# Kernel optimization log

Hardware: AMD Instinct MI355X
Metric: run time of the kernel (lower is better)

## Reference

```python
import jax, jax.numpy as jnp
import numpy as np

A = 9
H = 384
W = 384
MIN_SIZE = 2.0
NMS_THRESH = 0.7
PRE_NMS = 6000
POST_NMS = 300


def _make_anchors():
    # anchors.generate_anchors((H, W), box_sizes): per-cell (x1, y1, w, h) boxes in
    # feature-map coordinates, one box per (anchor, y, x).
    sizes = []
    for s in (4.0, 8.0, 16.0):
        for r in (0.5, 1.0, 2.0):
            sizes.append((s * np.sqrt(r), s / np.sqrt(r)))
    ys, xs = np.meshgrid(np.arange(H, dtype=np.float32), np.arange(W, dtype=np.float32), indexing='ij')
    cx, cy = xs + 0.5, ys + 0.5
    anch = np.stack([
        np.stack([cx - w / 2, cy - h / 2, np.full_like(cx, w), np.full_like(cx, h)], axis=-1)
        for (w, h) in sizes
    ], axis=0)  # [A, H, W, 4]
    return jnp.asarray(anch, jnp.float32)


def setup_inputs() -> dict:
    key = jax.random.key(0)
    k1, k2 = jax.random.split(key)
    scores = jax.random.uniform(k1, (1, A, H, W), dtype=jnp.float32)
    bbox_deltas = jax.random.normal(k2, (1, 4 * A, H, W), dtype=jnp.float32)
    return {
        'scores': scores,
        'bbox_deltas': bbox_deltas,
        'anchor_boxes': _make_anchors(),
        'image_metadata': jnp.zeros((1, 3), jnp.float32),
    }


def _clip_boxes(boxes, length, width):
    # clip_boxes_batch: clamp everything to >=0, convert (x,y,w,h)->(x1,y1,x2,y2),
    # clip to feature-map bounds, convert back.
    b = jnp.maximum(boxes, 0.0)
    x1, y1, w, h = b[..., 0], b[..., 1], b[..., 2], b[..., 3]
    x2 = x1 + w - 1.0
    y2 = y1 + h - 1.0
    x1 = jnp.minimum(x1, length - 1.0)
    y1 = jnp.minimum(y1, width - 1.0)
    x2 = jnp.minimum(x2, length - 1.0)
    y2 = jnp.minimum(y2, width - 1.0)
    return jnp.stack([x1, y1, x2 - x1 + 1.0, y2 - y1 + 1.0], axis=-1)


def _nms(boxes, valid):
    # Faithful port of the source's sequential NMS: repeatedly pick the remaining
    # box with the largest y2, suppress boxes whose intersection / own-area >= thresh.
    x1, y1, w, h = boxes[:, 0], boxes[:, 1], boxes[:, 2], boxes[:, 3]
    x2 = x1 + w - 1.0
    y2 = y1 + h - 1.0
    areas = w * h
    NEG = jnp.float32(-1e30)

    def cond(st):
        v, keep, cnt = st
        return (cnt < POST_NMS) & jnp.any(v)

    def body(st):
        v, keep, cnt = st
        ind = jnp.argmax(jnp.where(v, y2, NEG))
        xx1 = jnp.maximum(x1, x1[ind])
        yy1 = jnp.maximum(y1, y1[ind])
        xx2 = jnp.minimum(x2, x2[ind])
        yy2 = jnp.minimum(y2, y2[ind])
        inter = jnp.maximum(xx2 - xx1 + 1.0, 0.0) * jnp.maximum(yy2 - yy1 + 1.0, 0.0)
        ratio = inter / areas  # intersection over each candidate's own area (as in source)
        nv = v & (ratio < NMS_THRESH)
        nv = nv.at[ind].set(False)
        return nv, keep.at[cnt].set(ind.astype(jnp.int32)), cnt + 1

    keep0 = jnp.full((POST_NMS,), -1, jnp.int32)
    _, keep, cnt = jax.lax.while_loop(cond, body, (valid, keep0, jnp.int32(0)))
    return keep, cnt


def reference(scores, bbox_deltas, anchor_boxes, image_metadata):
    B = 1
    _, _, Hh, Ww = scores.shape
    # two contiguous .view()s compose to a single reshape
    deltas = bbox_deltas.reshape(B, A, Hh, Ww, 4)
    boxes = anchor_boxes[None] + deltas               # [1, A, H, W, 4]
    clipped = _clip_boxes(boxes, float(Hh), float(Ww))
    keep = (clipped[..., 2] >= MIN_SIZE) & (clipped[..., 3] >= MIN_SIZE)

    N = A * Hh * Ww
    boxes_f = clipped.reshape(N, 4)
    scores_f = scores.reshape(N)
    masked = jnp.where(keep.reshape(N), scores_f, jnp.float32(-jnp.inf))

    # descending score sort, PRE_NMS_TOP_N truncation
    order = jnp.argsort(-masked)[:PRE_NMS]
    props = boxes_f[order]                            # [PRE_NMS, 4]
    sc = masked[order]
    valid = jnp.isfinite(sc)

    keep_idx, cnt = _nms(props, valid)
    sel = props[jnp.maximum(keep_idx, 0)]             # [POST_NMS, 4]
    slot_valid = jnp.arange(POST_NMS) < cnt
    out = jnp.where(slot_valid[:, None], sel, 0.0)[None]  # [1, POST_NMS, 4]
    return out
```

## Files before the change

### kernel.cpp

```cpp
#include <hip/hip_runtime.h>
#include <stdint.h>

#define NN 1327104
#define NQ 331776
#define NB 1296
#define PRE_NMS_ 6000
#define POST_NMS_ 300
#define LB_CAP 4096
#define NPAD 6144
#define NWORD 96
#define KB 16
#define MATB 192


static __device__ __forceinline__ uint32_t score_key(float s) {
  uint32_t b = __float_as_uint(s);
  uint32_t u = b ^ (((int32_t)b < 0) ? 0xFFFFFFFFu : 0x80000000u);
  return ~u;
}

static __device__ __forceinline__ uint32_t f2s(float v) {
  uint32_t b = __float_as_uint(v);
  return b ^ (((int32_t)b < 0) ? 0xFFFFFFFFu : 0x80000000u);
}

static __device__ __forceinline__ void compute_box(float4 an, float4 de,
    float& x1, float& y1, float& wc, float& hc, bool& keep) {
  float bx = fmaxf(an.x + de.x, 0.0f);
  float by = fmaxf(an.y + de.y, 0.0f);
  float bw = fmaxf(an.z + de.z, 0.0f);
  float bh = fmaxf(an.w + de.w, 0.0f);
  float x2 = bx + bw - 1.0f;
  float y2 = by + bh - 1.0f;
  x1 = fminf(bx, 383.0f);
  y1 = fminf(by, 383.0f);
  x2 = fminf(x2, 383.0f);
  y2 = fminf(y2, 383.0f);
  wc = x2 - x1 + 1.0f;
  hc = y2 - y1 + 1.0f;
  keep = (wc >= 2.0f) && (hc >= 2.0f);
}

static __device__ __forceinline__ uint32_t kb18_of(float s) {
  return (uint32_t)(s * 262144.0f);
}

static __device__ __forceinline__ uint32_t wscan(uint32_t v, int l) {
  #pragma unroll
  for (int off = 1; off < 64; off <<= 1) {
    uint32_t u = __shfl_up(v, off);
    if (l >= off) v += u;
  }
  return v;
}

static __device__ __forceinline__ void pick1_f(const uint32_t* __restrict__ h1,
                                               uint32_t& selR8, uint32_t& base1) {
  int l = threadIdx.x & 63;
  uint32_t a0 = h1[l*5], a1 = h1[l*5+1], a2 = h1[l*5+2], a3 = h1[l*5+3], a4 = h1[l*5+4];
  uint32_t c0 = a0, c1 = c0+a1, c2 = c1+a2, c3 = c2+a3, c4 = c3+a4;
  uint32_t inc = wscan(c4, l);
  uint32_t excl = inc - c4;
  bool hit = (excl < PRE_NMS_) && (inc >= PRE_NMS_);
  unsigned long long hb = __ballot(hit);
  int hl = __ffsll(hb) - 1;
  uint32_t k, cb;
  if      (excl + c0 >= PRE_NMS_) { k = 0; cb = 0;  }
  else if (excl + c1 >= PRE_NMS_) { k = 1; cb = c0; }
  else if (excl + c2 >= PRE_NMS_) { k = 2; cb = c1; }
  else if (excl + c3 >= PRE_NMS_) { k = 3; cb = c2; }
  else                            { k = 4; cb = c3; }
  selR8 = __shfl(l*5u + k, hl);
  base1 = __shfl(excl + cb, hl);
}

static __device__ __forceinline__ void pick2_f(const uint32_t* __restrict__ h2,
                                               uint32_t base1,
                                               uint32_t& selR10, uint32_t& C0) {
  int l = threadIdx.x & 63;
  const uint4* p = (const uint4*)(h2 + l * 16);
  uint4 va = p[0], vb = p[1], vc = p[2], vd = p[3];
  uint32_t h[16] = {va.x,va.y,va.z,va.w, vb.x,vb.y,vb.z,vb.w,
                    vc.x,vc.y,vc.z,vc.w, vd.x,vd.y,vd.z,vd.w};
  uint32_t cum[16]; cum[0] = h[0];
  #pragma unroll
  for (int k = 1; k < 16; ++k) cum[k] = cum[k-1] + h[k];
  uint32_t inc = wscan(cum[15], l);
  uint32_t excl = base1 + inc - cum[15];
  bool hit = (excl < PRE_NMS_) && (base1 + inc >= PRE_NMS_);
  unsigned long long hb = __ballot(hit);
  int hl = __ffsll(hb) - 1;
  uint32_t k = 15, cb = cum[14];
  #pragma unroll
  for (int kk = 15; kk >= 0; --kk)
    if (excl + cum[kk] >= PRE_NMS_) { k = (uint32_t)kk; cb = kk ? cum[kk-1] : 0u; }
  selR10 = __shfl(l*16u + k, hl);
  C0 = __shfl(excl + cb, hl);
}

__global__ __launch_bounds__(256) void k_hA(const float* __restrict__ scores,
                                            const float4* __restrict__ deltas,
                                            const float4* __restrict__ anchors,
                                            uint32_t* __restrict__ darr,
                                            uint32_t* __restrict__ hist1,
                                            uint32_t* __restrict__ zpad) {
  __shared__ uint32_t lh[320];
  int t = threadIdx.x;
  for (int j = t; j < 320; j += 256) lh[j] = 0;
  __syncthreads();
  int base = blockIdx.x * 256 + t;
  #pragma unroll
  for (int it = 0; it < 4; ++it) {
    int i = base + it * NQ;
    float x1, y1, wc, hc; bool keep;
    compute_box(anchors[i], deltas[i], x1, y1, wc, hc, keep);
    float s = scores[i];
    uint32_t d = keep ? score_key(s) : 0xFF800000u;
    darr[i] = d;
    uint32_t r8 = keep ? (255u - (kb18_of(s) >> 10)) : 256u;
    atomicAdd(&lh[r8], 1u);
  }
  __syncthreads();
  for (int j = t; j < 320; j += 256) {
    uint32_t c = lh[j];
    if (c) atomicAdd(&hist1[j], c);
  }
  if (blockIdx.x == 0) for (int j = t; j < 1024 + 16 + 128; j += 256) zpad[j] = 0;
}

__global__ __launch_bounds__(256) void k_hB(const uint4* __restrict__ dv,
                                            const uint32_t* __restrict__ hist1,
                                            uint32_t* __restrict__ hist2) {
  __shared__ uint32_t lh2[1024];
  int t = threadIdx.x;
  uint32_t selR8, base1;
  pick1_f(hist1, selR8, base1);
  for (int j = t; j < 1024; j += 256) lh2[j] = 0;
  __syncthreads();
  uint4 v = dv[blockIdx.x * 256 + t];
  uint32_t arr[4] = {v.x, v.y, v.z, v.w};
  #pragma unroll
  for (int k = 0; k < 4; ++k) {
    uint32_t d = arr[k];
    if (d <= 0x7FFFFFFFu) {
      uint32_t kb = kb18_of(__uint_as_float(0x7FFFFFFFu - d));
      if ((255u - (kb >> 10)) == selR8) atomicAdd(&lh2[1023u - (kb & 1023u)], 1u);
    } else if (selR8 == 256u) {
      atomicAdd(&lh2[0], 1u);
    }
  }
  __syncthreads();
  for (int j = t; j < 1024; j += 256) {
    uint32_t c = lh2[j];
    if (c) atomicAdd(&hist2[j], c);
  }
}

__global__ __launch_bounds__(256) void k_gather(const uint4* __restrict__ dv,
                                                const uint32_t* __restrict__ hist1,
                                                const uint32_t* __restrict__ hist2,
                                                uint32_t* __restrict__ ctr,
                                                uint64_t* __restrict__ L,
                                                uint64_t* __restrict__ Lb) {
  __shared__ uint32_t s_sel8, s_sel10;
  int t = threadIdx.x;
  if (t < 64) {
    uint32_t sel8, base1, sel10, c0;
    pick1_f(hist1, sel8, base1);
    pick2_f(hist2, base1, sel10, c0);
    if (t == 0) { s_sel8 = sel8; s_sel10 = sel10; }
  }
  __syncthreads();
  uint32_t selR8 = s_sel8, selR10 = s_sel10;
  int g = blockIdx.x * 256 + t;
  uint4 v = dv[g];
  uint32_t arr[4] = {v.x, v.y, v.z, v.w};
  #pragma unroll
  for (int k = 0; k < 4; ++k) {
    uint32_t d = arr[k];
    uint32_t idx = (uint32_t)(g * 4 + k);
    bool above = false, boundary = false;
    if (d <= 0x7FFFFFFFu) {
      uint32_t kb = kb18_of(__uint_as_float(0x7FFFFFFFu - d));
      uint32_t r8 = 255u - (kb >> 10), r10 = 1023u - (kb & 1023u);
      above = (r8 < selR8) || (r8 == selR8 && r10 < selR10);
      boundary = (r8 == selR8) && (r10 == selR10);
    } else {
      boundary = (selR8 == 256u) && (selR10 == 0u);
    }
    if (above) {
      uint32_t p = atomicAdd(&ctr[0], 1u);
      if (p < PRE_NMS_) L[p] = ((uint64_t)d << 32) | idx;
    } else if (boundary) {
      uint32_t p = atomicAdd(&ctr[1], 1u);
      if (p < LB_CAP) Lb[p] = ((uint64_t)d << 32) | idx;
    }
  }
}

__global__ __launch_bounds__(256) void k_prep(const uint32_t* __restrict__ hist1,
                                              const uint32_t* __restrict__ hist2,
                                              const uint32_t* __restrict__ ctr,
                                              const uint64_t* __restrict__ L,
                                              const uint64_t* __restrict__ Lb,
                                              const float4* __restrict__ deltas,
                                              const float4* __restrict__ anchors,
                                              uint64_t* __restrict__ keyhi,
                                              uint32_t* __restrict__ keylo,
                                              float4* __restrict__ box4u) {
  uint32_t sel8, base1, sel10, C0;
  pick1_f(hist1, sel8, base1);
  pick2_f(hist2, base1, sel10, C0);
  int i = blockIdx.x * 256 + threadIdx.x;
  if (i >= NPAD) return;
  if (i < PRE_NMS_) {
    uint64_t mykey;
    if ((uint32_t)i < C0) {
      mykey = L[i];
    } else {
      uint32_t Cb = ctr[1]; if (Cb > LB_CAP) Cb = LB_CAP;
      uint32_t r = (uint32_t)i - C0;
      mykey = ~0ULL;
      for (uint32_t j = 0; j < Cb; ++j) {
        uint64_t kj = Lb[j];
        uint32_t rj = 0;
        for (uint32_t k = 0; k < Cb; ++k) rj += (Lb[k] < kj) ? 1u : 0u;
        if (rj == r) { mykey = kj; break; }
      }
    }
    uint32_t d = (uint32_t)(mykey >> 32), idx = (uint32_t)mykey;
    float x1, y1, wc, hc; bool keep;
    compute_box(anchors[idx], deltas[idx], x1, y1, wc, hc, keep);
    float y2 = y1 + hc - 1.0f;
    keyhi[i] = ((uint64_t)f2s(y2) << 32) | (uint32_t)(~d);
    keylo[i] = ~idx;
    box4u[i] = make_float4(x1, y1, wc, hc);
  } else {
    keyhi[i] = 0;
    keylo[i] = (uint32_t)(NPAD - i);
    box4u[i] = make_float4(0.f, 0.f, 0.f, 0.f);
  }
}

__global__ __launch_bounds__(512) void k_rank(const uint64_t* __restrict__ keyhi,
                                              const uint32_t* __restrict__ keylo,
                                              uint32_t* __restrict__ rank2d) {
  __shared__ uint64_t shi[768];
  __shared__ uint32_t slo[768];
  int t = threadIdx.x;
  int ib = blockIdx.x >> 3, c = blockIdx.x & 7, base = c * 768;
  for (int j = t; j < 768; j += 512) { shi[j] = keyhi[base + j]; slo[j] = keylo[base + j]; }
  __syncthreads();
  int i = ib * 256 + (t >> 1);
  int h = t & 1;
  uint64_t hi = keyhi[i]; uint32_t lo = keylo[i];
  uint32_t cnt = 0;
  int j0 = h * 384;
  for (int j = j0; j < j0 + 384; ++j) {
    uint64_t hj = shi[j]; uint32_t lj = slo[j];
    cnt += ((hj > hi) || (hj == hi && lj > lo)) ? 1u : 0u;
  }
  rank2d[i * 16 + c * 2 + h] = cnt;
}

#define FOR16(F) F(0) F(1) F(2) F(3) F(4) F(5) F(6) F(7) \
                 F(8) F(9) F(10) F(11) F(12) F(13) F(14) F(15)

static __device__ void seq_body(const unsigned long long* __restrict__ valid,
    const uint64_t* __restrict__ M, const float4* __restrict__ sobox,
    float* __restrict__ out, int* __restrict__ cslot) {
  int l = threadIdx.x;
  unsigned long long v0 = valid[l];
  unsigned long long v1 = (l < 32) ? valid[64 + l] : 0ull;
  uint32_t cnt = 0;

  for (;;) {
    uint32_t n0 = (uint32_t)__popcll(v0);
    uint32_t inc0 = wscan(n0, l);
    uint32_t T0 = __shfl(inc0, 63);
    uint32_t ex0 = inc0 - n0;
    uint32_t n1 = (uint32_t)__popcll(v1);
    uint32_t inc1 = wscan(n1, l);
    uint32_t T1 = __shfl(inc1, 63);
    uint32_t ex1 = T0 + inc1 - n1;
    uint32_t TV = T0 + T1;
    if (cnt >= POST_NMS_ || TV == 0) break;
    uint32_t m = (TV < KB) ? TV : KB;

    if (l < KB) cslot[l] = 0;
    __builtin_amdgcn_sched_barrier(0);
    if (ex0 < KB) {
      unsigned long long w = v0; uint32_t r = ex0;
      while (w && r < KB) { int b = __ffsll(w) - 1; cslot[r] = l * 64 + b; ++r; w &= w - 1; }
    }
    if (ex1 < KB && v1) {
      unsigned long long w = v1; uint32_t r = ex1;
      while (w && r < KB) { int b = __ffsll(w) - 1; cslot[r] = (64 + l) * 64 + b; ++r; w &= w - 1; }
    }
    __builtin_amdgcn_sched_barrier(0);

#define ROWDECL(k) uint64_t rm0_##k = 0, rm1_##k = 0;
    FOR16(ROWDECL)
#undef ROWDECL
#define ROWLOAD(k) if (k < (int)m) { const uint64_t* p = M + (size_t)cslot[k] * NWORD; \
                     rm0_##k = p[l]; rm1_##k = (l < 32) ? p[64 + l] : 0ull; }
    FOR16(ROWLOAD)
#undef ROWLOAD
    float4 obox = make_float4(0.f, 0.f, 0.f, 0.f);
    if (l < KB) obox = sobox[cslot[l]];

    uint32_t cj = (l < KB) ? (uint32_t)cslot[l] : 0u;
    uint32_t wj = cj >> 6, bj = cj & 63;
    int srcA = (int)(wj & 63), srcB = (int)(wj & 31);
    uint32_t srow[KB];
#define SROW(k) { uint64_t a = __shfl((unsigned long long)rm0_##k, srcA); \
                  uint64_t b = __shfl((unsigned long long)rm1_##k, srcB); \
                  uint64_t sel = (wj < 64) ? a : b; \
                  uint32_t bit = (l < KB && k < (int)m) ? (uint32_t)((sel >> bj) & 1) : 0u; \
                  srow[k] = (uint32_t)(__ballot(bit) & 0xFFFFull); }
    FOR16(SROW)
#undef SROW

    uint32_t cnt0 = cnt;
    uint32_t wm = 0, supp = 0;
    #pragma unroll
    for (int k = 0; k < KB; ++k) {
      if (k < (int)m && cnt < POST_NMS_ && !((supp >> k) & 1)) {
        wm |= 1u << k; ++cnt; supp |= srow[k];
      }
    }

    if (l < KB && ((wm >> l) & 1)) {
      uint32_t pos = cnt0 + (uint32_t)__popc(wm & ((1u << l) - 1));
      *(float4*)(out + (size_t)pos * 4) = obox;
    }

    uint64_t comb0 = 0, comb1 = 0;
#define COMB(k) if ((wm >> k) & 1) { comb0 |= rm0_##k; comb1 |= rm1_##k; }
    FOR16(COMB)
#undef COMB
    v0 &= ~comb0; v1 &= ~comb1;
  }

  for (int j = l; j < (int)(POST_NMS_ - cnt) * 4; j += 64) out[cnt * 4 + j] = 0.0f;
}

__global__ __launch_bounds__(512) void k_matsc(const uint64_t* __restrict__ keyhi,
                                               const uint32_t* __restrict__ rank2d,
                                               const float4* __restrict__ box4u,
                                               float4* __restrict__ sobox,
                                               unsigned long long* __restrict__ valid,
                                               uint64_t* __restrict__ M,
                                               uint32_t* __restrict__ ctr,
                                               float* __restrict__ out) {
  __shared__ float4 sb[NPAD];
  __shared__ float  sa[NPAD];
  __shared__ int    cslot[KB];
  __shared__ uint32_t lastf;
  int t = threadIdx.x;
  int b = blockIdx.x;
  for (int i = t; i < NPAD; i += 512) {
    const uint4* rp = (const uint4*)(rank2d + (size_t)i * 16);
    uint4 r0 = rp[0], r1 = rp[1], r2 = rp[2], r3 = rp[3];
    uint32_t r = r0.x+r0.y+r0.z+r0.w + r1.x+r1.y+r1.z+r1.w
               + r2.x+r2.y+r2.z+r2.w + r3.x+r3.y+r3.z+r3.w;
    float4 bx = box4u[i];
    float x2 = bx.x + bx.z - 1.0f;
    float y2 = bx.y + bx.w - 1.0f;
    sb[r] = make_float4(bx.x, bx.y, x2, y2);
    sa[r] = bx.z * bx.w;
    if (b == 0) {
      sobox[r] = bx;
      uint32_t d = ~(uint32_t)(keyhi[i] & 0xFFFFFFFFu);
      if (d < 0xFF800000u)
        atomicOr(&valid[r >> 6], 1ull << (r & 63));
    }
  }
  __syncthreads();
  int wid = t >> 6, l = t & 63;
  #pragma unroll
  for (int rr = 0; rr < 4; ++rr) {
    int r = b * 32 + wid * 4 + rr;
    float4 rb = sb[r];
    for (int w = 0; w < NWORD; ++w) {
      int j = w * 64 + l;
      float4 cb = sb[j];
      float ca = sa[j];
      float xx1 = fmaxf(cb.x, rb.x), yy1 = fmaxf(cb.y, rb.y);
      float xx2 = fminf(cb.z, rb.z), yy2 = fminf(cb.w, rb.w);
      float iw = fmaxf(xx2 - xx1 + 1.0f, 0.0f);
      float ih = fmaxf(yy2 - yy1 + 1.0f, 0.0f);
      float ratio = (iw * ih) / ca;
      unsigned long long mm = __ballot(!(ratio < 0.7f));
      if (l == 0) M[(size_t)r * NWORD + w] = mm;
    }
  }
  __syncthreads();
  __threadfence();
  if (t == 0) lastf = (atomicAdd(&ctr[8], 1u) == (uint32_t)(gridDim.x - 1)) ? 1u : 0u;
  __syncthreads();
  if (lastf) {
    __threadfence();
    if (t < 64) seq_body(valid, M, sobox, out, cslot);
  }
}

extern "C" void kernel_launch(void* const* d_in, const int* in_sizes, int n_in,
                              void* d_out, int out_size, void* d_ws, size_t ws_size,
                              hipStream_t stream) {
  const float*  scores  = (const float*)d_in[0];
  const float4* deltas  = (const float4*)d_in[1];
  const float4* anchors = (const float4*)d_in[2];
  float* out = (float*)d_out;

  uint8_t* w8 = (uint8_t*)d_ws;
  uint32_t* darr  = (uint32_t*)w8;
  uint64_t* M     = (uint64_t*)w8;
  float4*   sobox = (float4*)(w8 + 4841472);
  uint64_t* keyhi  = (uint64_t*)(w8 + 5308416);
  uint32_t* keylo  = (uint32_t*)(w8 + 5357568);
  float4*   box4u  = (float4*)  (w8 + 5382144);
  uint32_t* rank2d = (uint32_t*)(w8 + 5480448);
  uint32_t* hist1 = (uint32_t*)(w8 + 5873664);
  uint32_t* hist2 = (uint32_t*)(w8 + 5874944);
  uint32_t* ctr   = (uint32_t*)(w8 + 5879040);
  unsigned long long* valid = (unsigned long long*)(w8 + 5879104);
  uint64_t* L    = (uint64_t*)(w8 + 5880128);
  uint64_t* Lb   = (uint64_t*)(w8 + 5928128);

  const uint4* dv = (const uint4*)darr;

  hipMemsetAsync(hist1, 0, 1280, stream);

  k_hA    <<<NB, 256, 0, stream>>>(scores, deltas, anchors, darr, hist1, hist2);
  k_hB    <<<NB, 256, 0, stream>>>(dv, hist1, hist2);
  k_gather<<<NB, 256, 0, stream>>>(dv, hist1, hist2, ctr, L, Lb);
  k_prep  <<<NPAD / 256, 256, 0, stream>>>(hist1, hist2, ctr, L, Lb, deltas, anchors,
                                           keyhi, keylo, box4u);
  k_rank  <<<MATB, 512, 0, stream>>>(keyhi, keylo, rank2d);
  k_matsc <<<MATB, 512, 0, stream>>>(keyhi, rank2d, box4u, sobox, valid, M, ctr, out);
}
```

Measured before the change: 311.8 us.

## Fold second histogram pass and prep into gather, split sequential NMS kernel

Removes the second full-array histogram kernel and the separate prep kernel. The gather kernel now collects the whole 8-bit boundary bucket, and the last block builds the 10-bit histogram from that small list, picks the threshold, and emits keys and boxes directly. The quadratic rank search over the Lb list is replaced by a second-level select plus a small shared-memory rank among at most 256 items. The sequential NMS stage moves to its own 1024-thread kernel, where extra waves stream over the mask matrix to warm cache and the main wave raises its priority. The risks are a last-block serial tail, a larger boundary capacity whose overflow would give wrong results, and the bnd cap of 256.

```diff
diff --git a/kernel.cpp b/kernel.cpp
--- a/kernel.cpp
+++ b/kernel.cpp
@@ -6,7 +6,7 @@
 #define NB 1296
 #define PRE_NMS_ 6000
 #define POST_NMS_ 300
-#define LB_CAP 4096
+#define LB_CAP 16384
 #define NPAD 6144
 #define NWORD 96
 #define KB 16
@@ -74,28 +74,39 @@
   base1 = __shfl(excl + cb, hl);
 }
 
-static __device__ __forceinline__ void pick2_f(const uint32_t* __restrict__ h2,
-                                               uint32_t base1,
-                                               uint32_t& selR10, uint32_t& C0) {
+static __device__ __forceinline__ void pickT_lds(const uint32_t* __restrict__ h2,
+                                                 uint32_t T,
+                                                 uint32_t& sel10, uint32_t& base) {
   int l = threadIdx.x & 63;
-  const uint4* p = (const uint4*)(h2 + l * 16);
-  uint4 va = p[0], vb = p[1], vc = p[2], vd = p[3];
-  uint32_t h[16] = {va.x,va.y,va.z,va.w, vb.x,vb.y,vb.z,vb.w,
-                    vc.x,vc.y,vc.z,vc.w, vd.x,vd.y,vd.z,vd.w};
+  uint32_t h[16];
+  #pragma unroll
+  for (int k = 0; k < 16; ++k) h[k] = h2[l*16 + k];
   uint32_t cum[16]; cum[0] = h[0];
   #pragma unroll
   for (int k = 1; k < 16; ++k) cum[k] = cum[k-1] + h[k];
   uint32_t inc = wscan(cum[15], l);
-  uint32_t excl = base1 + inc - cum[15];
-  bool hit = (excl < PRE_NMS_) && (base1 + inc >= PRE_NMS_);
+  uint32_t excl = inc - cum[15];
+  bool hit = (excl < T) && (inc >= T);
   unsigned long long hb = __ballot(hit);
   int hl = __ffsll(hb) - 1;
   uint32_t k = 15, cb = cum[14];
   #pragma unroll
   for (int kk = 15; kk >= 0; --kk)
-    if (excl + cum[kk] >= PRE_NMS_) { k = (uint32_t)kk; cb = kk ? cum[kk-1] : 0u; }
-  selR10 = __shfl(l*16u + k, hl);
-  C0 = __shfl(excl + cb, hl);
+    if (excl + cum[kk] >= T) { k = (uint32_t)kk; cb = kk ? cum[kk-1] : 0u; }
+  sel10 = __shfl(l*16u + k, hl);
+  base  = __shfl(excl + cb, hl);
+}
+
+static __device__ __forceinline__ void emit_item(uint32_t pos, uint32_t d, uint32_t idx,
+    const float4* __restrict__ deltas, const float4* __restrict__ anchors,
+    uint64_t* __restrict__ keyhi, uint32_t* __restrict__ keylo,
+    float4* __restrict__ box4u) {
+  float x1, y1, wc, hc; bool keep;
+  compute_box(anchors[idx], deltas[idx], x1, y1, wc, hc, keep);
+  float y2 = y1 + hc - 1.0f;
+  keyhi[pos] = ((uint64_t)f2s(y2) << 32) | (uint32_t)(~d);
+  keylo[pos] = ~idx;
+  box4u[pos] = make_float4(x1, y1, wc, hc);
 }
 
 __global__ __launch_bounds__(256) void k_hA(const float* __restrict__ scores,
@@ -103,7 +114,7 @@
                                             const float4* __restrict__ anchors,
                                             uint32_t* __restrict__ darr,
                                             uint32_t* __restrict__ hist1,
-                                            uint32_t* __restrict__ zpad) {
+                                            uint32_t* __restrict__ zctr) {
   __shared__ uint32_t lh[320];
   int t = threadIdx.x;
   for (int j = t; j < 320; j += 256) lh[j] = 0;
@@ -125,53 +136,29 @@
     uint32_t c = lh[j];
     if (c) atomicAdd(&hist1[j], c);
   }
-  if (blockIdx.x == 0) for (int j = t; j < 1024 + 16 + 128; j += 256) zpad[j] = 0;
-}
-
-__global__ __launch_bounds__(256) void k_hB(const uint4* __restrict__ dv,
-                                            const uint32_t* __restrict__ hist1,
-                                            uint32_t* __restrict__ hist2) {
-  __shared__ uint32_t lh2[1024];
-  int t = threadIdx.x;
-  uint32_t selR8, base1;
-  pick1_f(hist1, selR8, base1);
-  for (int j = t; j < 1024; j += 256) lh2[j] = 0;
-  __syncthreads();
-  uint4 v = dv[blockIdx.x * 256 + t];
-  uint32_t arr[4] = {v.x, v.y, v.z, v.w};
-  #pragma unroll
-  for (int k = 0; k < 4; ++k) {
-    uint32_t d = arr[k];
-    if (d <= 0x7FFFFFFFu) {
-      uint32_t kb = kb18_of(__uint_as_float(0x7FFFFFFFu - d));
-      if ((255u - (kb >> 10)) == selR8) atomicAdd(&lh2[1023u - (kb & 1023u)], 1u);
-    } else if (selR8 == 256u) {
-      atomicAdd(&lh2[0], 1u);
-    }
-  }
-  __syncthreads();
-  for (int j = t; j < 1024; j += 256) {
-    uint32_t c = lh2[j];
-    if (c) atomicAdd(&hist2[j], c);
-  }
+  if (blockIdx.x == 0) for (int j = t; j < 272; j += 256) zctr[j] = 0;
 }
 
 __global__ __launch_bounds__(256) void k_gather(const uint4* __restrict__ dv,
                                                 const uint32_t* __restrict__ hist1,
-                                                const uint32_t* __restrict__ hist2,
                                                 uint32_t* __restrict__ ctr,
-                                                uint64_t* __restrict__ L,
-                                                uint64_t* __restrict__ Lb) {
-  __shared__ uint32_t s_sel8, s_sel10;
+                                                uint64_t* __restrict__ Lb,
+                                                uint64_t* __restrict__ keyhi,
+                                                uint32_t* __restrict__ keylo,
+                                                float4* __restrict__ box4u,
+                                                const float4* __restrict__ deltas,
+                                                const float4* __restrict__ anchors) {
+  __shared__ uint32_t s_sel8;
+  __shared__ uint32_t lastf;
   int t = threadIdx.x;
   if (t < 64) {
-    uint32_t sel8, base1, sel10, c0;
+    uint32_t sel8, base1;
     pick1_f(hist1, sel8, base1);
-    pick2_f(hist2, base1, sel10, c0);
-    if (t == 0) { s_sel8 = sel8; s_sel10 = sel10; }
-  }
-  __syncthreads();
-  uint32_t selR8 = s_sel8, selR10 = s_sel10;
+    if (t == 0) s_sel8 = sel8;
+  }
+  __syncthreads();
+  uint32_t selR8 = s_sel8;
+
   int g = blockIdx.x * 256 + t;
   uint4 v = dv[g];
   uint32_t arr[4] = {v.x, v.y, v.z, v.w};
@@ -179,66 +166,77 @@
   for (int k = 0; k < 4; ++k) {
     uint32_t d = arr[k];
     uint32_t idx = (uint32_t)(g * 4 + k);
-    bool above = false, boundary = false;
-    if (d <= 0x7FFFFFFFu) {
-      uint32_t kb = kb18_of(__uint_as_float(0x7FFFFFFFu - d));
-      uint32_t r8 = 255u - (kb >> 10), r10 = 1023u - (kb & 1023u);
-      above = (r8 < selR8) || (r8 == selR8 && r10 < selR10);
-      boundary = (r8 == selR8) && (r10 == selR10);
-    } else {
-      boundary = (selR8 == 256u) && (selR10 == 0u);
-    }
-    if (above) {
+    uint32_t r8 = (d <= 0x7FFFFFFFu)
+                ? (255u - (kb18_of(__uint_as_float(0x7FFFFFFFu - d)) >> 10)) : 256u;
+    if (r8 < selR8) {
       uint32_t p = atomicAdd(&ctr[0], 1u);
-      if (p < PRE_NMS_) L[p] = ((uint64_t)d << 32) | idx;
-    } else if (boundary) {
-      uint32_t p = atomicAdd(&ctr[1], 1u);
-      if (p < LB_CAP) Lb[p] = ((uint64_t)d << 32) | idx;
-    }
-  }
-}
-
-__global__ __launch_bounds__(256) void k_prep(const uint32_t* __restrict__ hist1,
-                                              const uint32_t* __restrict__ hist2,
-                                              const uint32_t* __restrict__ ctr,
-                                              const uint64_t* __restrict__ L,
-                                              const uint64_t* __restrict__ Lb,
-                                              const float4* __restrict__ deltas,
-                                              const float4* __restrict__ anchors,
-                                              uint64_t* __restrict__ keyhi,
-                                              uint32_t* __restrict__ keylo,
-                                              float4* __restrict__ box4u) {
-  uint32_t sel8, base1, sel10, C0;
-  pick1_f(hist1, sel8, base1);
-  pick2_f(hist2, base1, sel10, C0);
-  int i = blockIdx.x * 256 + threadIdx.x;
-  if (i >= NPAD) return;
-  if (i < PRE_NMS_) {
-    uint64_t mykey;
-    if ((uint32_t)i < C0) {
-      mykey = L[i];
-    } else {
-      uint32_t Cb = ctr[1]; if (Cb > LB_CAP) Cb = LB_CAP;
-      uint32_t r = (uint32_t)i - C0;
-      mykey = ~0ULL;
-      for (uint32_t j = 0; j < Cb; ++j) {
-        uint64_t kj = Lb[j];
-        uint32_t rj = 0;
-        for (uint32_t k = 0; k < Cb; ++k) rj += (Lb[k] < kj) ? 1u : 0u;
-        if (rj == r) { mykey = kj; break; }
-      }
-    }
-    uint32_t d = (uint32_t)(mykey >> 32), idx = (uint32_t)mykey;
-    float x1, y1, wc, hc; bool keep;
-    compute_box(anchors[idx], deltas[idx], x1, y1, wc, hc, keep);
-    float y2 = y1 + hc - 1.0f;
-    keyhi[i] = ((uint64_t)f2s(y2) << 32) | (uint32_t)(~d);
-    keylo[i] = ~idx;
-    box4u[i] = make_float4(x1, y1, wc, hc);
-  } else {
-    keyhi[i] = 0;
-    keylo[i] = (uint32_t)(NPAD - i);
-    box4u[i] = make_float4(0.f, 0.f, 0.f, 0.f);
+      if (p < PRE_NMS_) emit_item(p, d, idx, deltas, anchors, keyhi, keylo, box4u);
+    } else if (r8 == selR8) {
+      uint32_t q = atomicAdd(&ctr[1], 1u);
+      if (q < LB_CAP) Lb[q] = ((uint64_t)d << 32) | idx;
+    }
+  }
+
+  __threadfence();
+  if (t == 0) lastf = (atomicAdd(&ctr[9], 1u) == (uint32_t)(gridDim.x - 1)) ? 1u : 0u;
+  __syncthreads();
+  if (!lastf) return;
+  __threadfence();
+
+  __shared__ uint32_t lh2[1024];
+  __shared__ uint64_t bnd[256];
+  __shared__ uint32_t bcnt, lcnt, s_sel10, s_base;
+  for (int j = t; j < 1024; j += 256) lh2[j] = 0;
+  if (t == 0) { bcnt = 0; lcnt = 0; }
+  __syncthreads();
+
+  uint32_t C1 = ctr[0]; if (C1 > PRE_NMS_) C1 = PRE_NMS_;
+  uint32_t Cb = ctr[1]; if (Cb > LB_CAP) Cb = LB_CAP;
+  uint32_t T = PRE_NMS_ - C1;
+
+  for (uint32_t j = t; j < Cb; j += 256) {
+    uint32_t d = (uint32_t)(Lb[j] >> 32);
+    uint32_t r10 = (d <= 0x7FFFFFFFu)
+                 ? (1023u - (kb18_of(__uint_as_float(0x7FFFFFFFu - d)) & 1023u)) : 0u;
+    atomicAdd(&lh2[r10], 1u);
+  }
+  __syncthreads();
+  if (t < 64) {
+    uint32_t sel10 = 0xFFFFFFFFu, b2 = 0;
+    if (T > 0) pickT_lds(lh2, T, sel10, b2);
+    if (t == 0) { s_sel10 = sel10; s_base = b2; }
+  }
+  __syncthreads();
+  uint32_t sel10 = s_sel10, C2base = s_base;
+
+  for (uint32_t j = t; j < Cb; j += 256) {
+    uint64_t kj = Lb[j];
+    uint32_t d = (uint32_t)(kj >> 32), idx = (uint32_t)kj;
+    uint32_t r10 = (d <= 0x7FFFFFFFu)
+                 ? (1023u - (kb18_of(__uint_as_float(0x7FFFFFFFu - d)) & 1023u)) : 0u;
+    if (r10 < sel10) {
+      uint32_t p = C1 + atomicAdd(&lcnt, 1u);
+      if (p < PRE_NMS_) emit_item(p, d, idx, deltas, anchors, keyhi, keylo, box4u);
+    } else if (r10 == sel10) {
+      uint32_t q = atomicAdd(&bcnt, 1u);
+      if (q < 256) bnd[q] = kj;
+    }
+  }
+  __syncthreads();
+  uint32_t B = (bcnt < 256u) ? bcnt : 256u;
+  uint32_t T2 = (T > C2base) ? (T - C2base) : 0u;
+  for (uint32_t j = t; j < B; j += 256) {
+    uint64_t kj = bnd[j];
+    uint32_t r = 0;
+    for (uint32_t k = 0; k < B; ++k) r += (bnd[k] < kj) ? 1u : 0u;
+    if (r < T2)
+      emit_item(C1 + C2base + r, (uint32_t)(kj >> 32), (uint32_t)kj,
+                deltas, anchors, keyhi, keylo, box4u);
+  }
+  for (int j = PRE_NMS_ + t; j < NPAD; j += 256) {
+    keyhi[j] = 0;
+    keylo[j] = (uint32_t)(NPAD - j);
+    box4u[j] = make_float4(0.f, 0.f, 0.f, 0.f);
   }
 }
 
@@ -263,100 +261,14 @@
   rank2d[i * 16 + c * 2 + h] = cnt;
 }
 
-#define FOR16(F) F(0) F(1) F(2) F(3) F(4) F(5) F(6) F(7) \
-                 F(8) F(9) F(10) F(11) F(12) F(13) F(14) F(15)
-
-static __device__ void seq_body(const unsigned long long* __restrict__ valid,
-    const uint64_t* __restrict__ M, const float4* __restrict__ sobox,
-    float* __restrict__ out, int* __restrict__ cslot) {
-  int l = threadIdx.x;
-  unsigned long long v0 = valid[l];
-  unsigned long long v1 = (l < 32) ? valid[64 + l] : 0ull;
-  uint32_t cnt = 0;
-
-  for (;;) {
-    uint32_t n0 = (uint32_t)__popcll(v0);
-    uint32_t inc0 = wscan(n0, l);
-    uint32_t T0 = __shfl(inc0, 63);
-    uint32_t ex0 = inc0 - n0;
-    uint32_t n1 = (uint32_t)__popcll(v1);
-    uint32_t inc1 = wscan(n1, l);
-    uint32_t T1 = __shfl(inc1, 63);
-    uint32_t ex1 = T0 + inc1 - n1;
-    uint32_t TV = T0 + T1;
-    if (cnt >= POST_NMS_ || TV == 0) break;
-    uint32_t m = (TV < KB) ? TV : KB;
-
-    if (l < KB) cslot[l] = 0;
-    __builtin_amdgcn_sched_barrier(0);
-    if (ex0 < KB) {
-      unsigned long long w = v0; uint32_t r = ex0;
-      while (w && r < KB) { int b = __ffsll(w) - 1; cslot[r] = l * 64 + b; ++r; w &= w - 1; }
-    }
-    if (ex1 < KB && v1) {
-      unsigned long long w = v1; uint32_t r = ex1;
-      while (w && r < KB) { int b = __ffsll(w) - 1; cslot[r] = (64 + l) * 64 + b; ++r; w &= w - 1; }
-    }
-    __builtin_amdgcn_sched_barrier(0);
-
-#define ROWDECL(k) uint64_t rm0_##k = 0, rm1_##k = 0;
-    FOR16(ROWDECL)
-#undef ROWDECL
-#define ROWLOAD(k) if (k < (int)m) { const uint64_t* p = M + (size_t)cslot[k] * NWORD; \
-                     rm0_##k = p[l]; rm1_##k = (l < 32) ? p[64 + l] : 0ull; }
-    FOR16(ROWLOAD)
-#undef ROWLOAD
-    float4 obox = make_float4(0.f, 0.f, 0.f, 0.f);
-    if (l < KB) obox = sobox[cslot[l]];
-
-    uint32_t cj = (l < KB) ? (uint32_t)cslot[l] : 0u;
-    uint32_t wj = cj >> 6, bj = cj & 63;
-    int srcA = (int)(wj & 63), srcB = (int)(wj & 31);
-    uint32_t srow[KB];
-#define SROW(k) { uint64_t a = __shfl((unsigned long long)rm0_##k, srcA); \
-                  uint64_t b = __shfl((unsigned long long)rm1_##k, srcB); \
-                  uint64_t sel = (wj < 64) ? a : b; \
-                  uint32_t bit = (l < KB && k < (int)m) ? (uint32_t)((sel >> bj) & 1) : 0u; \
-                  srow[k] = (uint32_t)(__ballot(bit) & 0xFFFFull); }
-    FOR16(SROW)
-#undef SROW
-
-    uint32_t cnt0 = cnt;
-    uint32_t wm = 0, supp = 0;
-    #pragma unroll
-    for (int k = 0; k < KB; ++k) {
-      if (k < (int)m && cnt < POST_NMS_ && !((supp >> k) & 1)) {
-        wm |= 1u << k; ++cnt; supp |= srow[k];
-      }
-    }
-
-    if (l < KB && ((wm >> l) & 1)) {
-      uint32_t pos = cnt0 + (uint32_t)__popc(wm & ((1u << l) - 1));
-      *(float4*)(out + (size_t)pos * 4) = obox;
-    }
-
-    uint64_t comb0 = 0, comb1 = 0;
-#define COMB(k) if ((wm >> k) & 1) { comb0 |= rm0_##k; comb1 |= rm1_##k; }
-    FOR16(COMB)
-#undef COMB
-    v0 &= ~comb0; v1 &= ~comb1;
-  }
-
-  for (int j = l; j < (int)(POST_NMS_ - cnt) * 4; j += 64) out[cnt * 4 + j] = 0.0f;
-}
-
 __global__ __launch_bounds__(512) void k_matsc(const uint64_t* __restrict__ keyhi,
                                                const uint32_t* __restrict__ rank2d,
                                                const float4* __restrict__ box4u,
                                                float4* __restrict__ sobox,
                                                unsigned long long* __restrict__ valid,
-                                               uint64_t* __restrict__ M,
-                                               uint32_t* __restrict__ ctr,
-                                               float* __restrict__ out) {
+                                               uint64_t* __restrict__ M) {
   __shared__ float4 sb[NPAD];
   __shared__ float  sa[NPAD];
-  __shared__ int    cslot[KB];
-  __shared__ uint32_t lastf;
   int t = threadIdx.x;
   int b = blockIdx.x;
   for (int i = t; i < NPAD; i += 512) {
@@ -395,14 +307,102 @@
       if (l == 0) M[(size_t)r * NWORD + w] = mm;
     }
   }
-  __syncthreads();
-  __threadfence();
-  if (t == 0) lastf = (atomicAdd(&ctr[8], 1u) == (uint32_t)(gridDim.x - 1)) ? 1u : 0u;
-  __syncthreads();
-  if (lastf) {
-    __threadfence();
-    if (t < 64) seq_body(valid, M, sobox, out, cslot);
-  }
+}
+
+__global__ __launch_bounds__(1024) void k_seq(const unsigned long long* __restrict__ valid,
+                                              const uint64_t* __restrict__ M,
+                                              const float4* __restrict__ sobox,
+                                              float* __restrict__ out) {
+  int t = threadIdx.x;
+  if (t >= 64) {
+    const uint4* p = (const uint4*)M;
+    uint4 acc = make_uint4(0, 0, 0, 0);
+    for (int j = t - 64; j < 3072 * 24; j += 960) {
+      uint4 v = p[j];
+      acc.x ^= v.x; acc.y ^= v.y; acc.z ^= v.z; acc.w ^= v.w;
+    }
+    asm volatile("" :: "v"(acc.x), "v"(acc.y), "v"(acc.z), "v"(acc.w));
+    return;
+  }
+  __builtin_amdgcn_s_setprio(1);
+  int l = t;
+  unsigned long long v0 = valid[l];
+  unsigned long long v1 = (l < 32) ? valid[64 + l] : 0ull;
+  uint32_t cnt = 0;
+
+  for (;;) {
+    if (cnt >= POST_NMS_) break;
+    unsigned long long B0 = __ballot(v0 != 0ull);
+    unsigned long long B1 = __ballot((l < 32) && (v1 != 0ull));
+    if ((B0 | B1) == 0ull) break;
+
+    uint64_t p0 = 0, p1 = 0, p2 = 0, p3 = 0;
+    int m = 0;
+    while (m < KB && (B0 | B1)) {
+      int wsel; unsigned long long wv;
+      if (B0) { wsel = __ffsll(B0) - 1; B0 &= B0 - 1; wv = __shfl(v0, wsel); }
+      else    { int q = __ffsll(B1) - 1; wsel = 64 + q; B1 &= B1 - 1; wv = __shfl(v1, q); }
+      while (wv && m < KB) {
+        int bb = __ffsll(wv) - 1; wv &= wv - 1;
+        uint64_t ins = (uint64_t)(uint32_t)(wsel * 64 + bb) << ((m & 3) * 16);
+        if (m < 4) p0 |= ins; else if (m < 8) p1 |= ins;
+        else if (m < 12) p2 |= ins; else p3 |= ins;
+        ++m;
+      }
+    }
+#define SLOT(k) ((uint32_t)((((k) < 4 ? p0 : (k) < 8 ? p1 : (k) < 12 ? p2 : p3) \
+                             >> (((k) & 3) * 16)) & 0xFFFFu))
+#define FOR16(F) F(0) F(1) F(2) F(3) F(4) F(5) F(6) F(7) \
+                 F(8) F(9) F(10) F(11) F(12) F(13) F(14) F(15)
+
+#define ROWDECL(k) uint64_t rm0_##k = 0, rm1_##k = 0;
+    FOR16(ROWDECL)
+#undef ROWDECL
+#define ROWLOAD(k) if (k < m) { const uint64_t* rp = M + (size_t)SLOT(k) * NWORD; \
+                     rm0_##k = rp[l]; rm1_##k = (l < 32) ? rp[64 + l] : 0ull; }
+    FOR16(ROWLOAD)
+#undef ROWLOAD
+    uint64_t pkl = (l < 4) ? p0 : (l < 8) ? p1 : (l < 12) ? p2 : p3;
+    uint32_t cj = (uint32_t)((pkl >> ((l & 3) * 16)) & 0xFFFFu);
+    float4 obox = make_float4(0.f, 0.f, 0.f, 0.f);
+    if (l < KB) obox = sobox[cj];
+
+    uint32_t wj = cj >> 6, bj = cj & 63;
+    int srcA = (int)(wj & 63), srcB = (int)(wj & 31);
+    uint32_t srow[KB];
+#define SROW(k) { uint64_t a = __shfl((unsigned long long)rm0_##k, srcA); \
+                  uint64_t b = __shfl((unsigned long long)rm1_##k, srcB); \
+                  uint64_t sel = (wj < 64) ? a : b; \
+                  uint32_t bit = (l < KB && k < m) ? (uint32_t)((sel >> bj) & 1) : 0u; \
+                  srow[k] = (uint32_t)(__ballot(bit) & 0xFFFFull); }
+    FOR16(SROW)
+#undef SROW
+
+    uint32_t cnt0 = cnt;
+    uint32_t wm = 0, supp = 0;
+    #pragma unroll
+    for (int k = 0; k < KB; ++k) {
+      if (k < m && cnt < POST_NMS_ && !((supp >> k) & 1)) {
+        wm |= 1u << k; ++cnt; supp |= srow[k];
+      }
+    }
+
+    if (l < KB && ((wm >> l) & 1)) {
+      uint32_t pos = cnt0 + (uint32_t)__popc(wm & ((1u << l) - 1));
+      *(float4*)(out + (size_t)pos * 4) = obox;
+    }
+
+    uint64_t comb0 = 0, comb1 = 0;
+#define COMB(k) if ((wm >> k) & 1) { comb0 |= rm0_##k; comb1 |= rm1_##k; }
+    FOR16(COMB)
+#undef COMB
+#undef FOR16
+#undef SLOT
+    v0 &= ~comb0; v1 &= ~comb1;
+  }
+  __builtin_amdgcn_s_setprio(0);
+
+  for (int j = l; j < (int)(POST_NMS_ - cnt) * 4; j += 64) out[cnt * 4 + j] = 0.0f;
 }
 
 extern "C" void kernel_launch(void* const* d_in, const int* in_sizes, int n_in,
@@ -422,21 +422,18 @@
   float4*   box4u  = (float4*)  (w8 + 5382144);
   uint32_t* rank2d = (uint32_t*)(w8 + 5480448);
   uint32_t* hist1 = (uint32_t*)(w8 + 5873664);
-  uint32_t* hist2 = (uint32_t*)(w8 + 5874944);
-  uint32_t* ctr   = (uint32_t*)(w8 + 5879040);
-  unsigned long long* valid = (unsigned long long*)(w8 + 5879104);
-  uint64_t* L    = (uint64_t*)(w8 + 5880128);
-  uint64_t* Lb   = (uint64_t*)(w8 + 5928128);
+  uint32_t* ctr   = (uint32_t*)(w8 + 5874944);
+  unsigned long long* valid = (unsigned long long*)(w8 + 5875008);
+  uint64_t* Lb    = (uint64_t*)(w8 + 5876032);
 
   const uint4* dv = (const uint4*)darr;
 
   hipMemsetAsync(hist1, 0, 1280, stream);
 
-  k_hA    <<<NB, 256, 0, stream>>>(scores, deltas, anchors, darr, hist1, hist2);
-  k_hB    <<<NB, 256, 0, stream>>>(dv, hist1, hist2);
-  k_gather<<<NB, 256, 0, stream>>>(dv, hist1, hist2, ctr, L, Lb);
-  k_prep  <<<NPAD / 256, 256, 0, stream>>>(hist1, hist2, ctr, L, Lb, deltas, anchors,
-                                           keyhi, keylo, box4u);
+  k_hA    <<<NB, 256, 0, stream>>>(scores, deltas, anchors, darr, hist1, ctr);
+  k_gather<<<NB, 256, 0, stream>>>(dv, hist1, ctr, Lb, keyhi, keylo, box4u,
+                                   deltas, anchors);
   k_rank  <<<MATB, 512, 0, stream>>>(keyhi, keylo, rank2d);
-  k_matsc <<<MATB, 512, 0, stream>>>(keyhi, rank2d, box4u, sobox, valid, M, ctr, out);
-}
+  k_matsc <<<MATB, 512, 0, stream>>>(keyhi, rank2d, box4u, sobox, valid, M);
+  k_seq   <<<1, 1024, 0, stream>>>(valid, M, sobox, out);
+}
```

After: 407.3 us. 1.31x slower.
